# Performance work log

Measured on AMD Instinct MI355X. Metric: run time of the kernel, lower is better.

## Reference

```python
import jax, jax.numpy as jnp
import numpy as np

N_NODES = 50000
N_EDGES = 800000
NUM_FEATURES = 128
H1, H2, H3 = 256, 512, 256


def setup_inputs() -> dict:
    key = jax.random.key(0)
    ks = jax.random.split(key, 14)

    def lin(kw, fan_in, fan_out):
        # torch nn.Linear-style init, stored as [in, out] for x @ W
        bound = 1.0 / np.sqrt(fan_in)
        W = jax.random.uniform(kw, (fan_in, fan_out), jnp.float32, -bound, bound)
        b = jnp.zeros((fan_out,), jnp.float32)
        return W, b

    x = jax.random.normal(ks[0], (N_NODES, NUM_FEATURES), jnp.float32)
    edge_index = jax.random.randint(ks[1], (2, N_EDGES), 0, N_NODES, jnp.int64 if jax.config.jax_enable_x64 else jnp.int32)

    W1, b1 = lin(ks[2], NUM_FEATURES, H1)
    W2, b2 = lin(ks[3], H1, H2)
    W3, b3 = lin(ks[4], H2, H3)
    Wf1, bf1 = lin(ks[5], H3, 128)
    Wf2, bf2 = lin(ks[6], 128, 64)
    Wf3, bf3 = lin(ks[7], 64, 1)

    return {"x": x, "edge_index": edge_index,
            "W1": W1, "b1": b1, "W2": W2, "b2": b2, "W3": W3, "b3": b3,
            "Wf1": Wf1, "bf1": bf1, "Wf2": Wf2, "bf2": bf2, "Wf3": Wf3, "bf3": bf3}


def gcn_conv(x, W, b, row, col, dinv_row_col, n):
    # PyG GCNConv: out = D^{-1/2} (A+I) D^{-1/2} (x W) + b, self-loops already in row/col
    h = x @ W                              # [N, out]
    msg = h[row] * dinv_row_col[:, None]   # gather + edge-wise scale: [E+N, out]
    return jax.ops.segment_sum(msg, col, num_segments=n) + b


def reference(x, edge_index, W1, b1, W2, b2, W3, b3, Wf1, bf1, Wf2, bf2, Wf3, bf3):
    n = x.shape[0]
    loop = jnp.arange(n, dtype=edge_index.dtype)
    row = jnp.concatenate([edge_index[0], loop])   # sources (with self-loops)
    col = jnp.concatenate([edge_index[1], loop])   # targets (with self-loops)

    # symmetric normalization (computed once; identical for all three convs)
    deg = jax.ops.segment_sum(jnp.ones(col.shape[0], x.dtype), col, num_segments=n)
    dinv = jnp.where(deg > 0, jax.lax.rsqrt(deg), 0.0)
    norm = dinv[row] * dinv[col]                   # [E+N]

    h = jax.nn.relu(gcn_conv(x, W1, b1, row, col, norm, n))
    h = jax.nn.relu(gcn_conv(h, W2, b2, row, col, norm, n))
    h = jax.nn.relu(gcn_conv(h, W3, b3, row, col, norm, n))

    g = jnp.mean(h, axis=0, keepdims=True)         # [1, H3]
    g = jax.nn.relu(g @ Wf1 + bf1)
    g = jax.nn.relu(g @ Wf2 + bf2)
    return g @ Wf3 + bf3                           # [1, 1]
```

## Files before the change

### kernel.cpp

```cpp
#include <hip/hip_runtime.h>
#include <hip/hip_bf16.h>

#define N_NODES 50000
#define N_EDGES 800000
#define N_BUCKETS 64
#define M_PAD 50048
#define SCAN_NB 196

typedef short short8 __attribute__((ext_vector_type(8)));
typedef float floatx4 __attribute__((ext_vector_type(4)));
typedef float floatx2 __attribute__((ext_vector_type(2)));

__device__ __forceinline__ unsigned short f2bf(float f) {
    unsigned u = __float_as_uint(f);
    unsigned r = (u + 0x7fff + ((u >> 16) & 1)) >> 16;
    return (unsigned short)r;
}
__device__ __forceinline__ float bf2f(unsigned short h) {
    return __uint_as_float(((unsigned)h) << 16);
}
__device__ __forceinline__ void expand2(unsigned u, float& lo, float& hi) {
    lo = __uint_as_float(u << 16);
    hi = __uint_as_float(u & 0xffff0000u);
}

__device__ __forceinline__ unsigned pack4_fp8(float f0, float f1, float f2, float f3) {
    int v = __builtin_amdgcn_cvt_pk_fp8_f32(f0, f1, 0, false);
    v = __builtin_amdgcn_cvt_pk_fp8_f32(f2, f3, v, true);
    return (unsigned)v;
}
__device__ __forceinline__ void accum_fp8x4(float* a, unsigned u, float w) {
    floatx2 lo = __builtin_amdgcn_cvt_pk_f32_fp8((int)u, false);
    floatx2 hi = __builtin_amdgcn_cvt_pk_f32_fp8((int)u, true);
    a[0] += lo[0] * w; a[1] += lo[1] * w;
    a[2] += hi[0] * w; a[3] += hi[1] * w;
}
__device__ __forceinline__ void accum_fp8x2(float* a, unsigned u, float w) {
    floatx2 lo = __builtin_amdgcn_cvt_pk_f32_fp8((int)u, false);
    a[0] += lo[0] * w; a[1] += lo[1] * w;
}

__device__ __forceinline__ void gload16(const void* gp, void* lp) {
    __builtin_amdgcn_global_load_lds(
        (const __attribute__((address_space(1))) unsigned int*)gp,
        (__attribute__((address_space(3))) unsigned int*)lp,
        16, 0, 0);
}

__global__ void k_init(int* __restrict__ cnt, float* __restrict__ gb) {
    int i = blockIdx.x * blockDim.x + threadIdx.x;
    if (i < N_NODES) cnt[i] = 0;
    if (i < N_BUCKETS * 256) gb[i] = 0.0f;
}

__global__ void k_count(const int* __restrict__ col, int* __restrict__ cnt) {
    int e = blockIdx.x * blockDim.x + threadIdx.x;
    if (e < N_EDGES) atomicAdd(&cnt[col[e]], 1);
}

__global__ __launch_bounds__(256) void k_scanA(const int* __restrict__ cnt,
                                               int* __restrict__ bsum) {
    __shared__ int red[256];
    int t = threadIdx.x;
    int i = blockIdx.x * 256 + t;
    red[t] = (i < N_NODES) ? ((cnt[i] + 1) & ~1) : 0;
    __syncthreads();
    for (int d = 128; d > 0; d >>= 1) {
        if (t < d) red[t] += red[t + d];
        __syncthreads();
    }
    if (t == 0) bsum[blockIdx.x] = red[0];
}

__global__ __launch_bounds__(256) void k_scanB(const int* __restrict__ bsum,
                                               int* __restrict__ bbase,
                                               int* __restrict__ off) {
    __shared__ int sc[256];
    int t = threadIdx.x;
    sc[t] = (t < SCAN_NB) ? bsum[t] : 0;
    __syncthreads();
    for (int d = 1; d < 256; d <<= 1) {
        int v = 0;
        if (t >= d) v = sc[t - d];
        __syncthreads();
        if (t >= d) sc[t] += v;
        __syncthreads();
    }
    if (t < SCAN_NB) bbase[t] = sc[t] - bsum[t];
    if (t == SCAN_NB - 1) off[N_NODES] = sc[t];
}

__global__ __launch_bounds__(256) void k_scanC(const int* __restrict__ cnt,
                                               const int* __restrict__ bbase,
                                               int* __restrict__ off,
                                               int* __restrict__ cursor,
                                               float* __restrict__ dinv,
                                               int2* __restrict__ epack) {
    __shared__ int sc[256];
    int t = threadIdx.x;
    int i = blockIdx.x * 256 + t;
    int c = (i < N_NODES) ? cnt[i] : 0;
    int cap = (c + 1) & ~1;
    sc[t] = cap;
    __syncthreads();
    for (int d = 1; d < 256; d <<= 1) {
        int v = 0;
        if (t >= d) v = sc[t - d];
        __syncthreads();
        if (t >= d) sc[t] += v;
        __syncthreads();
    }
    if (i < N_NODES) {
        int excl = sc[t] - cap + bbase[blockIdx.x];
        off[i] = excl;
        cursor[i] = excl;
        dinv[i] = 1.0f / sqrtf((float)(c + 1));
        if (c & 1) epack[excl + c] = make_int2(i, 0);
    }
}

__global__ void k_fill(const int* __restrict__ row, const int* __restrict__ col,
                       const float* __restrict__ dinv, int* __restrict__ cursor,
                       int2* __restrict__ epack) {
    int e = blockIdx.x * blockDim.x + threadIdx.x;
    if (e >= N_EDGES) return;
    int v = col[e];
    int p = atomicAdd(&cursor[v], 1);
    int r = row[e];
    epack[p] = make_int2(r, __float_as_int(dinv[r]));
}

__global__ void k_prepW(const float* __restrict__ W,
                        unsigned short* __restrict__ Th,
                        unsigned short* __restrict__ Tl, int K, int N) {
    int idx = blockIdx.x * blockDim.x + threadIdx.x;
    if (idx >= K * N) return;
    int n = idx / K, k = idx - n * K;
    float v = W[(size_t)k * N + n];
    unsigned short h = f2bf(v);
    Th[idx] = h;
    Tl[idx] = f2bf(v - bf2f(h));
}

__global__ void k_prepX8(const float* __restrict__ x, unsigned char* __restrict__ xq) {
    int i = blockIdx.x * blockDim.x + threadIdx.x;
    if (i >= N_NODES * 32) return;
    const float* s = x + (size_t)i * 4;
    *(unsigned*)&xq[(size_t)i * 4] = pack4_fp8(s[0], s[1], s[2], s[3]);
}

template <int DIM, int POOL>
__global__ __launch_bounds__(256) void k_aggf(
    const unsigned char* __restrict__ xq, const int* __restrict__ off,
    const int2* __restrict__ epack, const float* __restrict__ dinv,
    const float* __restrict__ bias, unsigned short* __restrict__ outb,
    float* __restrict__ gb) {
    const int FPL = DIM / 64;
    __shared__ float gpart[256];
    if (POOL) {
        gpart[threadIdx.x] = 0.0f;
        __syncthreads();
    }
    int wv = threadIdx.x >> 6;
    int li = threadIdx.x & 63;
    int v = blockIdx.x * 4 + wv;
    int f = li * FPL;
    float dv = dinv[v];
    const unsigned char* __restrict__ xf = xq + f;
    float a0[FPL], a1[FPL], a2[FPL], a3[FPL];
#pragma unroll
    for (int i = 0; i < FPL; ++i) { a0[i] = 0.f; a1[i] = 0.f; a2[i] = 0.f; a3[i] = 0.f; }
    if (FPL == 4) {
        accum_fp8x4(a0, *(const unsigned*)&xf[(size_t)v * DIM], dv);
    } else {
        accum_fp8x2(a0, (unsigned)*(const unsigned short*)&xf[(size_t)v * DIM], dv);
    }
    int s = off[v], e = off[v + 1];
    int j = s;
    for (; j + 4 <= e; j += 4) {
        int4 d0 = *(const int4*)&epack[j];
        int4 d1 = *(const int4*)&epack[j + 2];
        if (FPL == 4) {
            unsigned g0 = *(const unsigned*)&xf[(size_t)d0.x * DIM];
            unsigned g1 = *(const unsigned*)&xf[(size_t)d0.z * DIM];
            unsigned g2 = *(const unsigned*)&xf[(size_t)d1.x * DIM];
            unsigned g3 = *(const unsigned*)&xf[(size_t)d1.z * DIM];
            accum_fp8x4(a0, g0, __int_as_float(d0.y));
            accum_fp8x4(a1, g1, __int_as_float(d0.w));
            accum_fp8x4(a2, g2, __int_as_float(d1.y));
            accum_fp8x4(a3, g3, __int_as_float(d1.w));
        } else {
            unsigned g0 = *(const unsigned short*)&xf[(size_t)d0.x * DIM];
            unsigned g1 = *(const unsigned short*)&xf[(size_t)d0.z * DIM];
            unsigned g2 = *(const unsigned short*)&xf[(size_t)d1.x * DIM];
            unsigned g3 = *(const unsigned short*)&xf[(size_t)d1.z * DIM];
            accum_fp8x2(a0, g0, __int_as_float(d0.y));
            accum_fp8x2(a1, g1, __int_as_float(d0.w));
            accum_fp8x2(a2, g2, __int_as_float(d1.y));
            accum_fp8x2(a3, g3, __int_as_float(d1.w));
        }
    }
    if (j < e) {
        int4 d0 = *(const int4*)&epack[j];
        if (FPL == 4) {
            unsigned g0 = *(const unsigned*)&xf[(size_t)d0.x * DIM];
            unsigned g1 = *(const unsigned*)&xf[(size_t)d0.z * DIM];
            accum_fp8x4(a0, g0, __int_as_float(d0.y));
            accum_fp8x4(a1, g1, __int_as_float(d0.w));
        } else {
            unsigned g0 = *(const unsigned short*)&xf[(size_t)d0.x * DIM];
            unsigned g1 = *(const unsigned short*)&xf[(size_t)d0.z * DIM];
            accum_fp8x2(a0, g0, __int_as_float(d0.y));
            accum_fp8x2(a1, g1, __int_as_float(d0.w));
        }
    }
    float acc[FPL];
#pragma unroll
    for (int i = 0; i < FPL; ++i)
        acc[i] = ((a0[i] + a1[i]) + (a2[i] + a3[i])) * dv;
    if (!POOL) {
        if (FPL == 4) {
            uint2 o;
            o.x = (unsigned)f2bf(acc[0]) | ((unsigned)f2bf(acc[1]) << 16);
            o.y = (unsigned)f2bf(acc[2]) | ((unsigned)f2bf(acc[3]) << 16);
            *(uint2*)&outb[(size_t)v * DIM + f] = o;
        } else {
            unsigned o = (unsigned)f2bf(acc[0]) | ((unsigned)f2bf(acc[1]) << 16);
            *(unsigned*)&outb[(size_t)v * DIM + f] = o;
        }
    } else {
#pragma unroll
        for (int i = 0; i < FPL; ++i) {
            float r = fmaxf(acc[i] + bias[f + i], 0.0f);
            atomicAdd(&gpart[f + i], r);
        }
        __syncthreads();
        atomicAdd(&gb[(blockIdx.x & (N_BUCKETS - 1)) * 256 + threadIdx.x],
                  gpart[threadIdx.x]);
    }
}

template <int BIAS, int RELU, int OUTFP8>
__global__ __launch_bounds__(256) void k_gemm_b(
    const unsigned short* __restrict__ A,
    const unsigned short* __restrict__ Bh, const unsigned short* __restrict__ Bl,
    const float* __restrict__ bias, void* __restrict__ Cout,
    int M, int K, int N) {
    __shared__ unsigned short smem[4 * 4096];
    unsigned short* As  = smem;
    unsigned short* BsH = smem + 4096;
    unsigned short* BsL = smem + 8192;
    int tid = threadIdx.x;
    int lane = tid & 63;
    int w = tid >> 6;
    int wr = w & 1, wc = w >> 1;
    int bm = blockIdx.x * 128, bn = blockIdx.y * 128;

    floatx4 acc[4][4];
    floatx4 zero = {0.f, 0.f, 0.f, 0.f};
#pragma unroll
    for (int t = 0; t < 4; ++t)
#pragma unroll
        for (int u = 0; u < 4; ++u) acc[t][u] = zero;

    int c0 = w * 2, c1 = c0 + 1;
    int srow = lane >> 2;
    int kg = ((lane & 3) - ((lane >> 3) & 3)) & 3;
    int kc = kg * 8;
    const unsigned short* Ap0 = A + (size_t)(bm + c0 * 16 + srow) * K + kc;
    const unsigned short* Ap1 = A + (size_t)(bm + c1 * 16 + srow) * K + kc;
    const unsigned short* Bh0 = Bh + (size_t)(bn + c0 * 16 + srow) * K + kc;
    const unsigned short* Bh1 = Bh + (size_t)(bn + c1 * 16 + srow) * K + kc;
    const unsigned short* Bl0 = Bl + (size_t)(bn + c0 * 16 + srow) * K + kc;
    const unsigned short* Bl1 = Bl + (size_t)(bn + c1 * 16 + srow) * K + kc;

    const int KT = K >> 5;
    int fr = lane & 15;
    int fq = lane >> 4;
    int cl = ((fq + (fr >> 1)) & 3) * 8;

    for (int kt = 0; kt < KT; ++kt) {
        int k0 = kt * 32;
        gload16(Ap0 + k0, As + c0 * 512);
        gload16(Ap1 + k0, As + c1 * 512);
        gload16(Bh0 + k0, BsH + c0 * 512);
        gload16(Bh1 + k0, BsH + c1 * 512);
        gload16(Bl0 + k0, BsL + c0 * 512);
        gload16(Bl1 + k0, BsL + c1 * 512);
        __syncthreads();
        short8 av[4], bhv[4], blv[4];
#pragma unroll
        for (int t = 0; t < 4; ++t) {
            av[t]  = *(const short8*)&As[(wr * 64 + t * 16 + fr) * 32 + cl];
            bhv[t] = *(const short8*)&BsH[(wc * 64 + t * 16 + fr) * 32 + cl];
            blv[t] = *(const short8*)&BsL[(wc * 64 + t * 16 + fr) * 32 + cl];
        }
#pragma unroll
        for (int t = 0; t < 4; ++t)
#pragma unroll
            for (int u = 0; u < 4; ++u) {
                acc[t][u] = __builtin_amdgcn_mfma_f32_16x16x32_bf16(av[t], bhv[u], acc[t][u], 0, 0, 0);
                acc[t][u] = __builtin_amdgcn_mfma_f32_16x16x32_bf16(av[t], blv[u], acc[t][u], 0, 0, 0);
            }
        __syncthreads();
    }

    unsigned short* cq = smem + w * 4096;
#pragma unroll
    for (int u = 0; u < 4; ++u) {
        int colq = u * 16 + fr;
        float bv = BIAS ? bias[bn + wc * 64 + colq] : 0.0f;
#pragma unroll
        for (int t = 0; t < 4; ++t) {
#pragma unroll
            for (int r = 0; r < 4; ++r) {
                float o = acc[t][u][r] + bv;
                if (RELU) o = fmaxf(o, 0.f);
                cq[(t * 16 + fq * 4 + r) * 64 + colq] = f2bf(o);
            }
        }
    }
    __syncthreads();
    int lr = tid >> 4;
    int lc = (tid & 15) * 8;
    int wcq = lc >> 6;
    int lcq = lc & 63;
#pragma unroll
    for (int i = 0; i < 8; ++i) {
        int rowt = i * 16 + lr;
        int wrq = rowt >> 6;
        const unsigned short* src =
            smem + (wrq + wcq * 2) * 4096 + (rowt & 63) * 64 + lcq;
        int rowg = bm + rowt;
        if (rowg < M) {
            if (!OUTFP8) {
                unsigned short* C = (unsigned short*)Cout;
                *(uint4*)&C[(size_t)rowg * N + bn + lc] = *(const uint4*)src;
            } else {
                uint4 b = *(const uint4*)src;
                float f0, f1, f2, f3, f4, f5, f6, f7;
                expand2(b.x, f0, f1); expand2(b.y, f2, f3);
                expand2(b.z, f4, f5); expand2(b.w, f6, f7);
                uint2 q;
                q.x = pack4_fp8(f0, f1, f2, f3);
                q.y = pack4_fp8(f4, f5, f6, f7);
                unsigned char* C8 = (unsigned char*)Cout;
                *(uint2*)&C8[(size_t)rowg * N + bn + lc] = q;
            }
        }
    }
}

__global__ void k_mlp(const float* __restrict__ gb,
                      const float* __restrict__ Wf1, const float* __restrict__ bf1,
                      const float* __restrict__ Wf2, const float* __restrict__ bf2,
                      const float* __restrict__ Wf3, const float* __restrict__ bf3,
                      float* __restrict__ out) {
    __shared__ float s0[256], s1[128], s2[64];
    int t = threadIdx.x;
    float sum = 0.0f;
    for (int b = 0; b < N_BUCKETS; ++b) sum += gb[b * 256 + t];
    s0[t] = sum * (1.0f / (float)N_NODES);
    __syncthreads();
    if (t < 128) {
        float a = bf1[t];
        for (int k = 0; k < 256; ++k) a += s0[k] * Wf1[k * 128 + t];
        s1[t] = fmaxf(a, 0.0f);
    }
    __syncthreads();
    if (t < 64) {
        float a = bf2[t];
        for (int k = 0; k < 128; ++k) a += s1[k] * Wf2[k * 64 + t];
        s2[t] = fmaxf(a, 0.0f);
    }
    __syncthreads();
    if (t == 0) {
        float a = bf3[0];
        for (int k = 0; k < 64; ++k) a += s2[k] * Wf3[k];
        out[0] = a;
    }
}

extern "C" void kernel_launch(void* const* d_in, const int* in_sizes, int n_in,
                              void* d_out, int out_size, void* d_ws, size_t ws_size,
                              hipStream_t stream) {
    const float* x  = (const float*)d_in[0];
    const int* ei   = (const int*)d_in[1];
    const float* W1 = (const float*)d_in[2];
    const float* b1 = (const float*)d_in[3];
    const float* W2 = (const float*)d_in[4];
    const float* b2 = (const float*)d_in[5];
    const float* W3 = (const float*)d_in[6];
    const float* b3 = (const float*)d_in[7];
    const float* Wf1 = (const float*)d_in[8];
    const float* bf1 = (const float*)d_in[9];
    const float* Wf2 = (const float*)d_in[10];
    const float* bf2 = (const float*)d_in[11];
    const float* Wf3 = (const float*)d_in[12];
    const float* bf3 = (const float*)d_in[13];
    float* out = (float*)d_out;

    char* p = (char*)d_ws;
    auto alloc = [&](size_t bytes) {
        void* r = (void*)p;
        p += (bytes + 255) & ~((size_t)255);
        return r;
    };
    int*   cnt    = (int*)  alloc(N_NODES * sizeof(int));
    int*   off    = (int*)  alloc((N_NODES + 1) * sizeof(int));
    int*   cursor = (int*)  alloc(N_NODES * sizeof(int));
    int*   bsum   = (int*)  alloc(SCAN_NB * sizeof(int));
    int*   bbase  = (int*)  alloc(SCAN_NB * sizeof(int));
    float* dinv   = (float*)alloc(N_NODES * sizeof(float));
    int2*  epack  = (int2*) alloc((size_t)(N_EDGES + N_NODES) * sizeof(int2));
    float* gb     = (float*)alloc(N_BUCKETS * 256 * sizeof(float));
    unsigned short* W1h = (unsigned short*)alloc(128 * 256 * 2);
    unsigned short* W1l = (unsigned short*)alloc(128 * 256 * 2);
    unsigned short* W2h = (unsigned short*)alloc(256 * 512 * 2);
    unsigned short* W2l = (unsigned short*)alloc(256 * 512 * 2);
    unsigned short* W3h = (unsigned short*)alloc(512 * 256 * 2);
    unsigned short* W3l = (unsigned short*)alloc(512 * 256 * 2);
    unsigned char*  xq  = (unsigned char*) alloc((size_t)N_NODES * 128);
    unsigned short* t0  = (unsigned short*)alloc((size_t)M_PAD * 128 * 2);
    unsigned char*  h1q = (unsigned char*) alloc((size_t)N_NODES * 256);
    unsigned short* t1  = (unsigned short*)alloc((size_t)M_PAD * 256 * 2);
    unsigned short* h2  = (unsigned short*)alloc((size_t)M_PAD * 512 * 2);
    unsigned char*  t2q = (unsigned char*) alloc((size_t)N_NODES * 256);

    const int* row = ei;
    const int* col = ei + N_EDGES;

    const int NB = (N_NODES + 255) / 256;
    const int EB = (N_EDGES + 255) / 256;

    k_init<<<NB, 256, 0, stream>>>(cnt, gb);
    k_count<<<EB, 256, 0, stream>>>(col, cnt);
    k_scanA<<<SCAN_NB, 256, 0, stream>>>(cnt, bsum);
    k_scanB<<<1, 256, 0, stream>>>(bsum, bbase, off);
    k_scanC<<<SCAN_NB, 256, 0, stream>>>(cnt, bbase, off, cursor, dinv, epack);
    k_fill<<<EB, 256, 0, stream>>>(row, col, dinv, cursor, epack);

    k_prepW<<<(128 * 256 + 255) / 256, 256, 0, stream>>>(W1, W1h, W1l, 128, 256);
    k_prepW<<<(256 * 512 + 255) / 256, 256, 0, stream>>>(W2, W2h, W2l, 256, 512);
    k_prepW<<<(512 * 256 + 255) / 256, 256, 0, stream>>>(W3, W3h, W3l, 512, 256);
    k_prepX8<<<(N_NODES * 32 + 255) / 256, 256, 0, stream>>>(x, xq);

    const int M = N_NODES;
    const int MB = (M + 127) / 128;

    k_aggf<128, 0><<<N_NODES / 4, 256, 0, stream>>>(
        xq, off, epack, dinv, nullptr, t0, nullptr);
    {
        dim3 grid(MB, 256 / 128);
        k_gemm_b<1, 1, 1><<<grid, 256, 0, stream>>>(t0, W1h, W1l, b1, h1q, M, 128, 256);
    }
    k_aggf<256, 0><<<N_NODES / 4, 256, 0, stream>>>(
        h1q, off, epack, dinv, nullptr, t1, nullptr);
    {
        dim3 grid(MB, 512 / 128);
        k_gemm_b<1, 1, 0><<<grid, 256, 0, stream>>>(t1, W2h, W2l, b2, h2, M, 256, 512);
    }
    {
        dim3 grid(MB, 256 / 128);
        k_gemm_b<0, 0, 1><<<grid, 256, 0, stream>>>(h2, W3h, W3l, nullptr, t2q, M, 512, 256);
    }
    k_aggf<256, 1><<<N_NODES / 4, 256, 0, stream>>>(
        t2q, off, epack, dinv, b3, nullptr, gb);

    k_mlp<<<1, 256, 0, stream>>>(gb, Wf1, bf1, Wf2, bf2, Wf3, bf3, out);
}
```

Baseline: 456.0 us.

## Split edge list across lane groups with wider fp8 gathers in aggregation

The aggregation kernel now splits each node's 64 lanes into four 16-lane groups. Each group walks a different slice of the edge list and gathers 16 or 8 fp8 bytes per lane with wide vector loads, and the partial sums are then combined with cross-lane shuffles. The CSR is padded to multiples of four entries, and the self-loop is stored explicitly in the padding, so the separate self term and most of the tail handling go away. The aim is fewer, wider memory transactions and more edges in flight per wave. The cost is more padding entries to write and read, extra shuffle reductions, and per-lane selects in the epilogue.

```diff
diff --git a/kernel.cpp b/kernel.cpp
--- a/kernel.cpp
+++ b/kernel.cpp
@@ -35,9 +35,15 @@
     a[0] += lo[0] * w; a[1] += lo[1] * w;
     a[2] += hi[0] * w; a[3] += hi[1] * w;
 }
-__device__ __forceinline__ void accum_fp8x2(float* a, unsigned u, float w) {
-    floatx2 lo = __builtin_amdgcn_cvt_pk_f32_fp8((int)u, false);
-    a[0] += lo[0] * w; a[1] += lo[1] * w;
+__device__ __forceinline__ void accum16(float* a, uint4 u, float w) {
+    accum_fp8x4(a + 0,  u.x, w);
+    accum_fp8x4(a + 4,  u.y, w);
+    accum_fp8x4(a + 8,  u.z, w);
+    accum_fp8x4(a + 12, u.w, w);
+}
+__device__ __forceinline__ void accum8(float* a, uint2 u, float w) {
+    accum_fp8x4(a + 0, u.x, w);
+    accum_fp8x4(a + 4, u.y, w);
 }
 
 __device__ __forceinline__ void gload16(const void* gp, void* lp) {
@@ -63,7 +69,7 @@
     __shared__ int red[256];
     int t = threadIdx.x;
     int i = blockIdx.x * 256 + t;
-    red[t] = (i < N_NODES) ? ((cnt[i] + 1) & ~1) : 0;
+    red[t] = (i < N_NODES) ? ((cnt[i] + 4) & ~3) : 0;
     __syncthreads();
     for (int d = 128; d > 0; d >>= 1) {
         if (t < d) red[t] += red[t + d];
@@ -100,7 +106,7 @@
     int t = threadIdx.x;
     int i = blockIdx.x * 256 + t;
     int c = (i < N_NODES) ? cnt[i] : 0;
-    int cap = (c + 1) & ~1;
+    int cap = (c + 4) & ~3;
     sc[t] = cap;
     __syncthreads();
     for (int d = 1; d < 256; d <<= 1) {
@@ -114,8 +120,11 @@
         int excl = sc[t] - cap + bbase[blockIdx.x];
         off[i] = excl;
         cursor[i] = excl;
-        dinv[i] = 1.0f / sqrtf((float)(c + 1));
-        if (c & 1) epack[excl + c] = make_int2(i, 0);
+        float di = 1.0f / sqrtf((float)(c + 1));
+        dinv[i] = di;
+        epack[excl + c] = make_int2(i, __float_as_int(di));
+        for (int p = c + 1; p < cap; ++p)
+            epack[excl + p] = make_int2(i, 0);
     }
 }
 
@@ -155,85 +164,95 @@
     const int2* __restrict__ epack, const float* __restrict__ dinv,
     const float* __restrict__ bias, unsigned short* __restrict__ outb,
     float* __restrict__ gb) {
-    const int FPL = DIM / 64;
+    const int F = DIM / 16;
     __shared__ float gpart[256];
-    if (POOL) {
+    if constexpr (POOL) {
         gpart[threadIdx.x] = 0.0f;
         __syncthreads();
     }
-    int wv = threadIdx.x >> 6;
-    int li = threadIdx.x & 63;
-    int v = blockIdx.x * 4 + wv;
-    int f = li * FPL;
-    float dv = dinv[v];
-    const unsigned char* __restrict__ xf = xq + f;
-    float a0[FPL], a1[FPL], a2[FPL], a3[FPL];
-#pragma unroll
-    for (int i = 0; i < FPL; ++i) { a0[i] = 0.f; a1[i] = 0.f; a2[i] = 0.f; a3[i] = 0.f; }
-    if (FPL == 4) {
-        accum_fp8x4(a0, *(const unsigned*)&xf[(size_t)v * DIM], dv);
+    const int wv = threadIdx.x >> 6;
+    const int li = threadIdx.x & 63;
+    const int g = li >> 4;
+    const int q = li & 15;
+    const int v = blockIdx.x * 4 + wv;
+    const float dv = dinv[v];
+    const unsigned char* __restrict__ xf = xq + q * F;
+    float acc[F];
+#pragma unroll
+    for (int i = 0; i < F; ++i) acc[i] = 0.0f;
+
+    int j = off[v];
+    const int e = off[v + 1];
+    for (; j + 16 <= e; j += 16) {
+        const int2* ep = epack + j + g * 4;
+        int4 dA = *(const int4*)ep;
+        int4 dB = *(const int4*)(ep + 2);
+        if constexpr (DIM == 256) {
+            uint4 g0 = *(const uint4*)&xf[(size_t)dA.x * DIM];
+            uint4 g1 = *(const uint4*)&xf[(size_t)dA.z * DIM];
+            uint4 g2 = *(const uint4*)&xf[(size_t)dB.x * DIM];
+            uint4 g3 = *(const uint4*)&xf[(size_t)dB.z * DIM];
+            accum16(acc, g0, __int_as_float(dA.y));
+            accum16(acc, g1, __int_as_float(dA.w));
+            accum16(acc, g2, __int_as_float(dB.y));
+            accum16(acc, g3, __int_as_float(dB.w));
+        } else {
+            uint2 g0 = *(const uint2*)&xf[(size_t)dA.x * DIM];
+            uint2 g1 = *(const uint2*)&xf[(size_t)dA.z * DIM];
+            uint2 g2 = *(const uint2*)&xf[(size_t)dB.x * DIM];
+            uint2 g3 = *(const uint2*)&xf[(size_t)dB.z * DIM];
+            accum8(acc, g0, __int_as_float(dA.y));
+            accum8(acc, g1, __int_as_float(dA.w));
+            accum8(acc, g2, __int_as_float(dB.y));
+            accum8(acc, g3, __int_as_float(dB.w));
+        }
+    }
+    for (; j < e; j += 4) {
+        int2 d = epack[j + g];
+        if constexpr (DIM == 256) {
+            uint4 g0 = *(const uint4*)&xf[(size_t)d.x * DIM];
+            accum16(acc, g0, __int_as_float(d.y));
+        } else {
+            uint2 g0 = *(const uint2*)&xf[(size_t)d.x * DIM];
+            accum8(acc, g0, __int_as_float(d.y));
+        }
+    }
+
+#pragma unroll
+    for (int i = 0; i < F; ++i) {
+        float t = acc[i];
+        t += __shfl_xor(t, 16);
+        t += __shfl_xor(t, 32);
+        acc[i] = t * dv;
+    }
+
+    if constexpr (!POOL) {
+        if constexpr (DIM == 256) {
+            float o0 = g == 0 ? acc[0] : g == 1 ? acc[4] : g == 2 ? acc[8]  : acc[12];
+            float o1 = g == 0 ? acc[1] : g == 1 ? acc[5] : g == 2 ? acc[9]  : acc[13];
+            float o2 = g == 0 ? acc[2] : g == 1 ? acc[6] : g == 2 ? acc[10] : acc[14];
+            float o3 = g == 0 ? acc[3] : g == 1 ? acc[7] : g == 2 ? acc[11] : acc[15];
+            uint2 o;
+            o.x = (unsigned)f2bf(o0) | ((unsigned)f2bf(o1) << 16);
+            o.y = (unsigned)f2bf(o2) | ((unsigned)f2bf(o3) << 16);
+            *(uint2*)&outb[(size_t)v * DIM + q * 16 + g * 4] = o;
+        } else {
+            float o0 = g == 0 ? acc[0] : g == 1 ? acc[2] : g == 2 ? acc[4] : acc[6];
+            float o1 = g == 0 ? acc[1] : g == 1 ? acc[3] : g == 2 ? acc[5] : acc[7];
+            unsigned o = (unsigned)f2bf(o0) | ((unsigned)f2bf(o1) << 16);
+            *(unsigned*)&outb[(size_t)v * DIM + q * 8 + g * 2] = o;
+        }
     } else {
-        accum_fp8x2(a0, (unsigned)*(const unsigned short*)&xf[(size_t)v * DIM], dv);
-    }
-    int s = off[v], e = off[v + 1];
-    int j = s;
-    for (; j + 4 <= e; j += 4) {
-        int4 d0 = *(const int4*)&epack[j];
-        int4 d1 = *(const int4*)&epack[j + 2];
-        if (FPL == 4) {
-            unsigned g0 = *(const unsigned*)&xf[(size_t)d0.x * DIM];
-            unsigned g1 = *(const unsigned*)&xf[(size_t)d0.z * DIM];
-            unsigned g2 = *(const unsigned*)&xf[(size_t)d1.x * DIM];
-            unsigned g3 = *(const unsigned*)&xf[(size_t)d1.z * DIM];
-            accum_fp8x4(a0, g0, __int_as_float(d0.y));
-            accum_fp8x4(a1, g1, __int_as_float(d0.w));
-            accum_fp8x4(a2, g2, __int_as_float(d1.y));
-            accum_fp8x4(a3, g3, __int_as_float(d1.w));
-        } else {
-            unsigned g0 = *(const unsigned short*)&xf[(size_t)d0.x * DIM];
-            unsigned g1 = *(const unsigned short*)&xf[(size_t)d0.z * DIM];
-            unsigned g2 = *(const unsigned short*)&xf[(size_t)d1.x * DIM];
-            unsigned g3 = *(const unsigned short*)&xf[(size_t)d1.z * DIM];
-            accum_fp8x2(a0, g0, __int_as_float(d0.y));
-            accum_fp8x2(a1, g1, __int_as_float(d0.w));
-            accum_fp8x2(a2, g2, __int_as_float(d1.y));
-            accum_fp8x2(a3, g3, __int_as_float(d1.w));
-        }
-    }
-    if (j < e) {
-        int4 d0 = *(const int4*)&epack[j];
-        if (FPL == 4) {
-            unsigned g0 = *(const unsigned*)&xf[(size_t)d0.x * DIM];
-            unsigned g1 = *(const unsigned*)&xf[(size_t)d0.z * DIM];
-            accum_fp8x4(a0, g0, __int_as_float(d0.y));
-            accum_fp8x4(a1, g1, __int_as_float(d0.w));
-        } else {
-            unsigned g0 = *(const unsigned short*)&xf[(size_t)d0.x * DIM];
-            unsigned g1 = *(const unsigned short*)&xf[(size_t)d0.z * DIM];
-            accum_fp8x2(a0, g0, __int_as_float(d0.y));
-            accum_fp8x2(a1, g1, __int_as_float(d0.w));
-        }
-    }
-    float acc[FPL];
-#pragma unroll
-    for (int i = 0; i < FPL; ++i)
-        acc[i] = ((a0[i] + a1[i]) + (a2[i] + a3[i])) * dv;
-    if (!POOL) {
-        if (FPL == 4) {
-            uint2 o;
-            o.x = (unsigned)f2bf(acc[0]) | ((unsigned)f2bf(acc[1]) << 16);
-            o.y = (unsigned)f2bf(acc[2]) | ((unsigned)f2bf(acc[3]) << 16);
-            *(uint2*)&outb[(size_t)v * DIM + f] = o;
-        } else {
-            unsigned o = (unsigned)f2bf(acc[0]) | ((unsigned)f2bf(acc[1]) << 16);
-            *(unsigned*)&outb[(size_t)v * DIM + f] = o;
-        }
-    } else {
-#pragma unroll
-        for (int i = 0; i < FPL; ++i) {
-            float r = fmaxf(acc[i] + bias[f + i], 0.0f);
-            atomicAdd(&gpart[f + i], r);
-        }
+        float o0 = g == 0 ? acc[0] : g == 1 ? acc[4] : g == 2 ? acc[8]  : acc[12];
+        float o1 = g == 0 ? acc[1] : g == 1 ? acc[5] : g == 2 ? acc[9]  : acc[13];
+        float o2 = g == 0 ? acc[2] : g == 1 ? acc[6] : g == 2 ? acc[10] : acc[14];
+        float o3 = g == 0 ? acc[3] : g == 1 ? acc[7] : g == 2 ? acc[11] : acc[15];
+        const int fb = q * 16 + g * 4;
+        floatx4 bv = *(const floatx4*)&bias[fb];
+        atomicAdd(&gpart[fb + 0], fmaxf(o0 + bv[0], 0.0f));
+        atomicAdd(&gpart[fb + 1], fmaxf(o1 + bv[1], 0.0f));
+        atomicAdd(&gpart[fb + 2], fmaxf(o2 + bv[2], 0.0f));
+        atomicAdd(&gpart[fb + 3], fmaxf(o3 + bv[3], 0.0f));
         __syncthreads();
         atomicAdd(&gb[(blockIdx.x & (N_BUCKETS - 1)) * 256 + threadIdx.x],
                   gpart[threadIdx.x]);
@@ -412,7 +431,7 @@
     int*   bsum   = (int*)  alloc(SCAN_NB * sizeof(int));
     int*   bbase  = (int*)  alloc(SCAN_NB * sizeof(int));
     float* dinv   = (float*)alloc(N_NODES * sizeof(float));
-    int2*  epack  = (int2*) alloc((size_t)(N_EDGES + N_NODES) * sizeof(int2));
+    int2*  epack  = (int2*) alloc((size_t)(N_EDGES + 4 * N_NODES) * sizeof(int2));
     float* gb     = (float*)alloc(N_BUCKETS * 256 * sizeof(float));
     unsigned short* W1h = (unsigned short*)alloc(128 * 256 * 2);
     unsigned short* W1l = (unsigned short*)alloc(128 * 256 * 2);
```

Result: no change. 459.1 us (+0.7%).

## Slice CSR by source range and aggregate 13 destinations per wave for gather locality

Applied to the files above, without the earlier changes.

Builds the CSR over (destination, source-slice) cells, with 8 slices of 6250 source nodes each. The aggregation kernel is rewritten so each wave owns 13 consecutive destinations and walks all of their edges slice by slice. The aim is to keep the gathered source feature rows within one slice cache-resident across waves. The cost is a scan over 400K cells instead of 50K, separate self-loop kernels, more accumulator registers, and a scalar edge loop with no unroll or int4 edge loads, which may reduce occupancy and memory-level parallelism.

```diff
diff --git a/kernel.cpp b/kernel.cpp
--- a/kernel.cpp
+++ b/kernel.cpp
@@ -5,7 +5,14 @@
 #define N_EDGES 800000
 #define N_BUCKETS 64
 #define M_PAD 50048
-#define SCAN_NB 196
+
+#define NS 8
+#define SLICE_DIV 6250
+#define NC (N_NODES * NS)
+#define AGG_BLOCKS 1024
+#define NWAVES (AGG_BLOCKS * 4)
+#define DPW 13
+#define CELL_NB ((NC + 255) / 256)
 
 typedef short short8 __attribute__((ext_vector_type(8)));
 typedef float floatx4 __attribute__((ext_vector_type(4)));
@@ -47,23 +54,40 @@
         16, 0, 0);
 }
 
-__global__ void k_init(int* __restrict__ cnt, float* __restrict__ gb) {
+__global__ void k_init2(int* __restrict__ cnt2, float* __restrict__ gb) {
     int i = blockIdx.x * blockDim.x + threadIdx.x;
-    if (i < N_NODES) cnt[i] = 0;
+    if (i < NC) cnt2[i] = 0;
     if (i < N_BUCKETS * 256) gb[i] = 0.0f;
 }
 
-__global__ void k_count(const int* __restrict__ col, int* __restrict__ cnt) {
+__global__ void k_count2(const int* __restrict__ row, const int* __restrict__ col,
+                         int* __restrict__ cnt2) {
     int e = blockIdx.x * blockDim.x + threadIdx.x;
-    if (e < N_EDGES) atomicAdd(&cnt[col[e]], 1);
-}
-
-__global__ __launch_bounds__(256) void k_scanA(const int* __restrict__ cnt,
-                                               int* __restrict__ bsum) {
+    if (e >= N_EDGES) return;
+    int s = row[e] / SLICE_DIV;
+    atomicAdd(&cnt2[col[e] * NS + s], 1);
+}
+
+__global__ void k_self(int* __restrict__ cnt2) {
+    int i = blockIdx.x * blockDim.x + threadIdx.x;
+    if (i < N_NODES) atomicAdd(&cnt2[i * NS + i / SLICE_DIV], 1);
+}
+
+__global__ void k_dinv(const int* __restrict__ cnt2, float* __restrict__ dinv) {
+    int i = blockIdx.x * blockDim.x + threadIdx.x;
+    if (i >= N_NODES) return;
+    const int4* c4 = (const int4*)&cnt2[i * NS];
+    int4 a = c4[0], b = c4[1];
+    int c = a.x + a.y + a.z + a.w + b.x + b.y + b.z + b.w;
+    dinv[i] = 1.0f / sqrtf((float)c);
+}
+
+__global__ __launch_bounds__(256) void k_scanA2(const int* __restrict__ cnt2,
+                                                int* __restrict__ bsum) {
     __shared__ int red[256];
     int t = threadIdx.x;
     int i = blockIdx.x * 256 + t;
-    red[t] = (i < N_NODES) ? ((cnt[i] + 1) & ~1) : 0;
+    red[t] = (i < NC) ? cnt2[i] : 0;
     __syncthreads();
     for (int d = 128; d > 0; d >>= 1) {
         if (t < d) red[t] += red[t + d];
@@ -72,12 +96,41 @@
     if (t == 0) bsum[blockIdx.x] = red[0];
 }
 
-__global__ __launch_bounds__(256) void k_scanB(const int* __restrict__ bsum,
-                                               int* __restrict__ bbase,
-                                               int* __restrict__ off) {
+__global__ __launch_bounds__(256) void k_scanB2(const int* __restrict__ bsum,
+                                                int* __restrict__ bbase) {
+    __shared__ int sc[256];
+    __shared__ int carry;
+    int t = threadIdx.x;
+    if (t == 0) carry = 0;
+    __syncthreads();
+    for (int base = 0; base < CELL_NB; base += 256) {
+        int idx = base + t;
+        int v = (idx < CELL_NB) ? bsum[idx] : 0;
+        sc[t] = v;
+        __syncthreads();
+        for (int d = 1; d < 256; d <<= 1) {
+            int x = 0;
+            if (t >= d) x = sc[t - d];
+            __syncthreads();
+            if (t >= d) sc[t] += x;
+            __syncthreads();
+        }
+        if (idx < CELL_NB) bbase[idx] = carry + sc[t] - v;
+        __syncthreads();
+        if (t == 255) carry += sc[255];
+        __syncthreads();
+    }
+}
+
+__global__ __launch_bounds__(256) void k_scanC2(const int* __restrict__ cnt2,
+                                                const int* __restrict__ bbase,
+                                                int* __restrict__ off2,
+                                                int* __restrict__ cursor2) {
     __shared__ int sc[256];
     int t = threadIdx.x;
-    sc[t] = (t < SCAN_NB) ? bsum[t] : 0;
+    int i = blockIdx.x * 256 + t;
+    int c = (i < NC) ? cnt2[i] : 0;
+    sc[t] = c;
     __syncthreads();
     for (int d = 1; d < 256; d <<= 1) {
         int v = 0;
@@ -86,48 +139,32 @@
         if (t >= d) sc[t] += v;
         __syncthreads();
     }
-    if (t < SCAN_NB) bbase[t] = sc[t] - bsum[t];
-    if (t == SCAN_NB - 1) off[N_NODES] = sc[t];
-}
-
-__global__ __launch_bounds__(256) void k_scanC(const int* __restrict__ cnt,
-                                               const int* __restrict__ bbase,
-                                               int* __restrict__ off,
-                                               int* __restrict__ cursor,
-                                               float* __restrict__ dinv,
-                                               int2* __restrict__ epack) {
-    __shared__ int sc[256];
-    int t = threadIdx.x;
-    int i = blockIdx.x * 256 + t;
-    int c = (i < N_NODES) ? cnt[i] : 0;
-    int cap = (c + 1) & ~1;
-    sc[t] = cap;
-    __syncthreads();
-    for (int d = 1; d < 256; d <<= 1) {
-        int v = 0;
-        if (t >= d) v = sc[t - d];
-        __syncthreads();
-        if (t >= d) sc[t] += v;
-        __syncthreads();
-    }
-    if (i < N_NODES) {
-        int excl = sc[t] - cap + bbase[blockIdx.x];
-        off[i] = excl;
-        cursor[i] = excl;
-        dinv[i] = 1.0f / sqrtf((float)(c + 1));
-        if (c & 1) epack[excl + c] = make_int2(i, 0);
-    }
-}
-
-__global__ void k_fill(const int* __restrict__ row, const int* __restrict__ col,
-                       const float* __restrict__ dinv, int* __restrict__ cursor,
-                       int2* __restrict__ epack) {
+    if (i < NC) {
+        int o = sc[t] - c + bbase[blockIdx.x];
+        off2[i] = o;
+        cursor2[i] = o;
+        if (i == NC - 1) off2[NC] = o + c;
+    }
+}
+
+__global__ void k_fill2(const int* __restrict__ row, const int* __restrict__ col,
+                        const float* __restrict__ dinv, int* __restrict__ cursor2,
+                        int2* __restrict__ epack) {
     int e = blockIdx.x * blockDim.x + threadIdx.x;
     if (e >= N_EDGES) return;
+    int r = row[e];
     int v = col[e];
-    int p = atomicAdd(&cursor[v], 1);
-    int r = row[e];
+    int s = r / SLICE_DIV;
+    int p = atomicAdd(&cursor2[v * NS + s], 1);
     epack[p] = make_int2(r, __float_as_int(dinv[r]));
+}
+
+__global__ void k_fillself(const float* __restrict__ dinv, int* __restrict__ cursor2,
+                           int2* __restrict__ epack) {
+    int i = blockIdx.x * blockDim.x + threadIdx.x;
+    if (i >= N_NODES) return;
+    int p = atomicAdd(&cursor2[i * NS + i / SLICE_DIV], 1);
+    epack[p] = make_int2(i, __float_as_int(dinv[i]));
 }
 
 __global__ void k_prepW(const float* __restrict__ W,
@@ -150,93 +187,80 @@
 }
 
 template <int DIM, int POOL>
-__global__ __launch_bounds__(256) void k_aggf(
-    const unsigned char* __restrict__ xq, const int* __restrict__ off,
+__global__ __launch_bounds__(256) void k_aggp(
+    const unsigned char* __restrict__ xq, const int* __restrict__ off2,
     const int2* __restrict__ epack, const float* __restrict__ dinv,
     const float* __restrict__ bias, unsigned short* __restrict__ outb,
     float* __restrict__ gb) {
     const int FPL = DIM / 64;
-    __shared__ float gpart[256];
-    if (POOL) {
-        gpart[threadIdx.x] = 0.0f;
-        __syncthreads();
-    }
-    int wv = threadIdx.x >> 6;
-    int li = threadIdx.x & 63;
-    int v = blockIdx.x * 4 + wv;
-    int f = li * FPL;
-    float dv = dinv[v];
-    const unsigned char* __restrict__ xf = xq + f;
-    float a0[FPL], a1[FPL], a2[FPL], a3[FPL];
-#pragma unroll
-    for (int i = 0; i < FPL; ++i) { a0[i] = 0.f; a1[i] = 0.f; a2[i] = 0.f; a3[i] = 0.f; }
-    if (FPL == 4) {
-        accum_fp8x4(a0, *(const unsigned*)&xf[(size_t)v * DIM], dv);
+    const int wv = __builtin_amdgcn_readfirstlane(threadIdx.x >> 6);
+    const int li = threadIdx.x & 63;
+    const int wid = blockIdx.x * 4 + wv;
+    const int d0 = wid * DPW;
+    const unsigned char* __restrict__ xl = xq + li * FPL;
+
+    float acc[DPW][FPL];
+#pragma unroll
+    for (int di = 0; di < DPW; ++di)
+#pragma unroll
+        for (int i = 0; i < FPL; ++i) acc[di][i] = 0.0f;
+
+    for (int s = 0; s < NS; ++s) {
+#pragma unroll
+        for (int di = 0; di < DPW; ++di) {
+            int v = d0 + di;
+            if (v >= N_NODES) continue;
+            int cell = v * NS + s;
+            int jb = off2[cell];
+            int je = off2[cell + 1];
+            for (int j = jb; j < je; ++j) {
+                int2 ed = epack[j];
+                float w = __int_as_float(ed.y);
+                if constexpr (DIM == 256) {
+                    unsigned g = *(const unsigned*)&xl[(size_t)ed.x * DIM];
+                    accum_fp8x4(acc[di], g, w);
+                } else {
+                    unsigned g = (unsigned)*(const unsigned short*)&xl[(size_t)ed.x * DIM];
+                    accum_fp8x2(acc[di], g, w);
+                }
+            }
+        }
+    }
+
+    if constexpr (!POOL) {
+#pragma unroll
+        for (int di = 0; di < DPW; ++di) {
+            int v = d0 + di;
+            if (v >= N_NODES) continue;
+            float dv = dinv[v];
+            if constexpr (DIM == 256) {
+                uint2 o;
+                o.x = (unsigned)f2bf(acc[di][0] * dv) | ((unsigned)f2bf(acc[di][1] * dv) << 16);
+                o.y = (unsigned)f2bf(acc[di][2] * dv) | ((unsigned)f2bf(acc[di][3] * dv) << 16);
+                *(uint2*)&outb[(size_t)v * DIM + li * 4] = o;
+            } else {
+                unsigned o = (unsigned)f2bf(acc[di][0] * dv) | ((unsigned)f2bf(acc[di][1] * dv) << 16);
+                *(unsigned*)&outb[(size_t)v * DIM + li * 2] = o;
+            }
+        }
     } else {
-        accum_fp8x2(a0, (unsigned)*(const unsigned short*)&xf[(size_t)v * DIM], dv);
-    }
-    int s = off[v], e = off[v + 1];
-    int j = s;
-    for (; j + 4 <= e; j += 4) {
-        int4 d0 = *(const int4*)&epack[j];
-        int4 d1 = *(const int4*)&epack[j + 2];
-        if (FPL == 4) {
-            unsigned g0 = *(const unsigned*)&xf[(size_t)d0.x * DIM];
-            unsigned g1 = *(const unsigned*)&xf[(size_t)d0.z * DIM];
-            unsigned g2 = *(const unsigned*)&xf[(size_t)d1.x * DIM];
-            unsigned g3 = *(const unsigned*)&xf[(size_t)d1.z * DIM];
-            accum_fp8x4(a0, g0, __int_as_float(d0.y));
-            accum_fp8x4(a1, g1, __int_as_float(d0.w));
-            accum_fp8x4(a2, g2, __int_as_float(d1.y));
-            accum_fp8x4(a3, g3, __int_as_float(d1.w));
-        } else {
-            unsigned g0 = *(const unsigned short*)&xf[(size_t)d0.x * DIM];
-            unsigned g1 = *(const unsigned short*)&xf[(size_t)d0.z * DIM];
-            unsigned g2 = *(const unsigned short*)&xf[(size_t)d1.x * DIM];
-            unsigned g3 = *(const unsigned short*)&xf[(size_t)d1.z * DIM];
-            accum_fp8x2(a0, g0, __int_as_float(d0.y));
-            accum_fp8x2(a1, g1, __int_as_float(d0.w));
-            accum_fp8x2(a2, g2, __int_as_float(d1.y));
-            accum_fp8x2(a3, g3, __int_as_float(d1.w));
-        }
-    }
-    if (j < e) {
-        int4 d0 = *(const int4*)&epack[j];
-        if (FPL == 4) {
-            unsigned g0 = *(const unsigned*)&xf[(size_t)d0.x * DIM];
-            unsigned g1 = *(const unsigned*)&xf[(size_t)d0.z * DIM];
-            accum_fp8x4(a0, g0, __int_as_float(d0.y));
-            accum_fp8x4(a1, g1, __int_as_float(d0.w));
-        } else {
-            unsigned g0 = *(const unsigned short*)&xf[(size_t)d0.x * DIM];
-            unsigned g1 = *(const unsigned short*)&xf[(size_t)d0.z * DIM];
-            accum_fp8x2(a0, g0, __int_as_float(d0.y));
-            accum_fp8x2(a1, g1, __int_as_float(d0.w));
-        }
-    }
-    float acc[FPL];
-#pragma unroll
-    for (int i = 0; i < FPL; ++i)
-        acc[i] = ((a0[i] + a1[i]) + (a2[i] + a3[i])) * dv;
-    if (!POOL) {
-        if (FPL == 4) {
-            uint2 o;
-            o.x = (unsigned)f2bf(acc[0]) | ((unsigned)f2bf(acc[1]) << 16);
-            o.y = (unsigned)f2bf(acc[2]) | ((unsigned)f2bf(acc[3]) << 16);
-            *(uint2*)&outb[(size_t)v * DIM + f] = o;
-        } else {
-            unsigned o = (unsigned)f2bf(acc[0]) | ((unsigned)f2bf(acc[1]) << 16);
-            *(unsigned*)&outb[(size_t)v * DIM + f] = o;
-        }
-    } else {
-#pragma unroll
-        for (int i = 0; i < FPL; ++i) {
-            float r = fmaxf(acc[i] + bias[f + i], 0.0f);
-            atomicAdd(&gpart[f + i], r);
-        }
-        __syncthreads();
-        atomicAdd(&gb[(blockIdx.x & (N_BUCKETS - 1)) * 256 + threadIdx.x],
-                  gpart[threadIdx.x]);
+        floatx4 bv = *(const floatx4*)&bias[li * 4];
+        float ps0 = 0.f, ps1 = 0.f, ps2 = 0.f, ps3 = 0.f;
+#pragma unroll
+        for (int di = 0; di < DPW; ++di) {
+            int v = d0 + di;
+            if (v >= N_NODES) continue;
+            float dv = dinv[v];
+            ps0 += fmaxf(acc[di][0] * dv + bv[0], 0.0f);
+            ps1 += fmaxf(acc[di][1] * dv + bv[1], 0.0f);
+            ps2 += fmaxf(acc[di][2] * dv + bv[2], 0.0f);
+            ps3 += fmaxf(acc[di][3] * dv + bv[3], 0.0f);
+        }
+        float* g0 = &gb[(wid & (N_BUCKETS - 1)) * 256 + li * 4];
+        atomicAdd(g0 + 0, ps0);
+        atomicAdd(g0 + 1, ps1);
+        atomicAdd(g0 + 2, ps2);
+        atomicAdd(g0 + 3, ps3);
     }
 }
 
@@ -406,14 +430,14 @@
         p += (bytes + 255) & ~((size_t)255);
         return r;
     };
-    int*   cnt    = (int*)  alloc(N_NODES * sizeof(int));
-    int*   off    = (int*)  alloc((N_NODES + 1) * sizeof(int));
-    int*   cursor = (int*)  alloc(N_NODES * sizeof(int));
-    int*   bsum   = (int*)  alloc(SCAN_NB * sizeof(int));
-    int*   bbase  = (int*)  alloc(SCAN_NB * sizeof(int));
-    float* dinv   = (float*)alloc(N_NODES * sizeof(float));
-    int2*  epack  = (int2*) alloc((size_t)(N_EDGES + N_NODES) * sizeof(int2));
-    float* gb     = (float*)alloc(N_BUCKETS * 256 * sizeof(float));
+    int*   cnt2    = (int*)  alloc((size_t)NC * sizeof(int));
+    int*   off2    = (int*)  alloc((size_t)(NC + 1) * sizeof(int));
+    int*   cursor2 = (int*)  alloc((size_t)NC * sizeof(int));
+    int*   bsum2   = (int*)  alloc(CELL_NB * sizeof(int));
+    int*   bbase2  = (int*)  alloc(CELL_NB * sizeof(int));
+    float* dinv    = (float*)alloc(N_NODES * sizeof(float));
+    int2*  epack   = (int2*) alloc((size_t)(N_EDGES + N_NODES) * sizeof(int2));
+    float* gb      = (float*)alloc(N_BUCKETS * 256 * sizeof(float));
     unsigned short* W1h = (unsigned short*)alloc(128 * 256 * 2);
     unsigned short* W1l = (unsigned short*)alloc(128 * 256 * 2);
     unsigned short* W2h = (unsigned short*)alloc(256 * 512 * 2);
@@ -433,12 +457,15 @@
     const int NB = (N_NODES + 255) / 256;
     const int EB = (N_EDGES + 255) / 256;
 
-    k_init<<<NB, 256, 0, stream>>>(cnt, gb);
-    k_count<<<EB, 256, 0, stream>>>(col, cnt);
-    k_scanA<<<SCAN_NB, 256, 0, stream>>>(cnt, bsum);
-    k_scanB<<<1, 256, 0, stream>>>(bsum, bbase, off);
-    k_scanC<<<SCAN_NB, 256, 0, stream>>>(cnt, bbase, off, cursor, dinv, epack);
-    k_fill<<<EB, 256, 0, stream>>>(row, col, dinv, cursor, epack);
+    k_init2<<<CELL_NB, 256, 0, stream>>>(cnt2, gb);
+    k_count2<<<EB, 256, 0, stream>>>(row, col, cnt2);
+    k_self<<<NB, 256, 0, stream>>>(cnt2);
+    k_dinv<<<NB, 256, 0, stream>>>(cnt2, dinv);
+    k_scanA2<<<CELL_NB, 256, 0, stream>>>(cnt2, bsum2);
+    k_scanB2<<<1, 256, 0, stream>>>(bsum2, bbase2);
+    k_scanC2<<<CELL_NB, 256, 0, stream>>>(cnt2, bbase2, off2, cursor2);
+    k_fill2<<<EB, 256, 0, stream>>>(row, col, dinv, cursor2, epack);
+    k_fillself<<<NB, 256, 0, stream>>>(dinv, cursor2, epack);
 
     k_prepW<<<(128 * 256 + 255) / 256, 256, 0, stream>>>(W1, W1h, W1l, 128, 256);
     k_prepW<<<(256 * 512 + 255) / 256, 256, 0, stream>>>(W2, W2h, W2l, 256, 512);
@@ -448,14 +475,14 @@
     const int M = N_NODES;
     const int MB = (M + 127) / 128;
 
-    k_aggf<128, 0><<<N_NODES / 4, 256, 0, stream>>>(
-        xq, off, epack, dinv, nullptr, t0, nullptr);
+    k_aggp<128, 0><<<AGG_BLOCKS, 256, 0, stream>>>(
+        xq, off2, epack, dinv, nullptr, t0, nullptr);
     {
         dim3 grid(MB, 256 / 128);
         k_gemm_b<1, 1, 1><<<grid, 256, 0, stream>>>(t0, W1h, W1l, b1, h1q, M, 128, 256);
     }
-    k_aggf<256, 0><<<N_NODES / 4, 256, 0, stream>>>(
-        h1q, off, epack, dinv, nullptr, t1, nullptr);
+    k_aggp<256, 0><<<AGG_BLOCKS, 256, 0, stream>>>(
+        h1q, off2, epack, dinv, nullptr, t1, nullptr);
     {
         dim3 grid(MB, 512 / 128);
         k_gemm_b<1, 1, 0><<<grid, 256, 0, stream>>>(t1, W2h, W2l, b2, h2, M, 256, 512);
@@ -464,8 +491,8 @@
         dim3 grid(MB, 256 / 128);
         k_gemm_b<0, 0, 1><<<grid, 256, 0, stream>>>(h2, W3h, W3l, nullptr, t2q, M, 512, 256);
     }
-    k_aggf<256, 1><<<N_NODES / 4, 256, 0, stream>>>(
-        t2q, off, epack, dinv, b3, nullptr, gb);
+    k_aggp<256, 1><<<AGG_BLOCKS, 256, 0, stream>>>(
+        t2q, off2, epack, dinv, b3, nullptr, gb);
 
     k_mlp<<<1, 256, 0, stream>>>(gb, Wf1, bf1, Wf2, bf2, Wf3, bf3, out);
 }
```

Measured after the change: 629.8 us. 38.1% more time.
